# Performance work log

Hardware: AMD Instinct MI355X
Metric: run time of the kernel (lower is better)

## Reference

```python
import jax, jax.numpy as jnp
import numpy as np

N = 50000      # query points
M = 50000      # support points
KNN = 32       # neighbors per query
K = 15         # kernel points
C_IN = 64
C_OUT = 128
RADIUS = 2.5
KP_EXTENT = 1.2


def setup_inputs() -> dict:
    key = jax.random.key(0)
    ks = jax.random.split(key, 6)
    q_pts = jax.random.uniform(ks[0], (N, 3), dtype=jnp.float32)
    s_pts = jax.random.uniform(ks[1], (M, 3), dtype=jnp.float32)
    s_feats = jax.random.normal(ks[2], (M, C_IN), dtype=jnp.float32)
    # index M refers to the appended shadow point/feature row
    neigh_inds = jax.random.randint(ks[3], (N, KNN), 0, M + 1, dtype=jnp.int32)
    weights = jax.random.normal(ks[4], (K, C_IN, C_OUT), dtype=jnp.float32) * 0.05
    kernel_points = (jax.random.uniform(ks[5], (K, 3), dtype=jnp.float32) * 2.0 - 1.0) * RADIUS
    return {"q_pts": q_pts, "s_pts": s_pts, "s_feats": s_feats,
            "neigh_inds": neigh_inds, "weights": weights,
            "kernel_points": kernel_points}


def reference(q_pts, s_pts, s_feats, neigh_inds, weights, kernel_points):
    # append shadow point far away and zero shadow feature row
    s_pts_pad = jnp.concatenate([s_pts, jnp.full((1, 3), 1e6, s_pts.dtype)], axis=0)
    s_feats_pad = jnp.concatenate(
        [s_feats, jnp.zeros((1, s_feats.shape[1]), s_feats.dtype)], axis=0)

    neigh_pts = s_pts_pad[neigh_inds] - q_pts[:, None, :]       # (n, k, 3)
    neigh_feats = s_feats_pad[neigh_inds]                        # (n, k, c_in)

    diff = neigh_pts[:, :, None, :] - kernel_points[None, None]  # (n, k, K, 3)
    sq_dist = jnp.sum(diff * diff, axis=-1) + 1e-8               # (n, k, K)

    # linear kernel-point influence
    h = jnp.clip(1.0 - jnp.sqrt(sq_dist) / KP_EXTENT, 0.0)       # (n, k, K)

    # aggregate neighbor feats per kernel point, then apply per-kernel weights
    kernel_feats = jnp.einsum('nke,nkc->nec', h, neigh_feats)    # (n, K, c_in)
    q_feats = jnp.einsum('nec,eco->no', kernel_feats, weights)   # (n, c_out)

    # normalize by number of valid (non-shadow, sum>0) neighbors
    neighbor_num = jnp.sum(jnp.sum(neigh_feats, axis=-1) > 0, axis=-1)
    neighbor_num = jnp.maximum(neighbor_num, 1).astype(q_feats.dtype)[:, None]
    return q_feats / neighbor_num
```

## Files before the change

### kernel.cpp

```cpp
#include <hip/hip_runtime.h>


namespace {
constexpr int NQ   = 50000;
constexpr int MS   = 50000;
constexpr int KNN  = 32;
constexpr int KP   = 15;
constexpr int CIN  = 64;
constexpr int COUT = 128;
constexpr int QB   = 16;
constexpr int ROWS = KP * CIN;
constexpr int RND  = 3;
constexpr int RE   = 5;
constexpr int RROWS = RE * CIN;
constexpr int KBR  = RROWS / 32;
constexpr int KBT  = ROWS / 32;
constexpr int NT   = COUT / 16;
constexpr int ASTR = RROWS + 4;
constexpr float KP_EXT_INV = 1.0f / 1.2f;
constexpr size_t WS_HI  = 200704;
constexpr size_t WS_LO  = WS_HI + (size_t)ROWS * COUT * 2;
constexpr size_t WS_NEED = WS_LO + (size_t)ROWS * COUT * 2;
}

typedef __attribute__((ext_vector_type(8))) short short8;
typedef __attribute__((ext_vector_type(4))) float f32x4;

__device__ __forceinline__ short f32_bf16(float x) {
    unsigned u = __builtin_bit_cast(unsigned, x);
    u = u + 0x7fffu + ((u >> 16) & 1u);
    return (short)(u >> 16);
}
__device__ __forceinline__ float bf16_f32(short h) {
    unsigned u = ((unsigned)(unsigned short)h) << 16;
    return __builtin_bit_cast(float, u);
}

__global__ __launch_bounds__(256)
void rowsum_kernel(const float* __restrict__ s_feats, float* __restrict__ rs)
{
    int t = blockIdx.x * 256 + threadIdx.x;
    int row = t >> 3;
    int l8  = t & 7;
    if (row >= MS) return;
    const float4* p = (const float4*)(s_feats + (size_t)row * CIN + l8 * 8);
    float4 a = p[0], b = p[1];
    float s = ((a.x + a.y) + (a.z + a.w)) + ((b.x + b.y) + (b.z + b.w));
    s += __shfl_xor(s, 1);
    s += __shfl_xor(s, 2);
    s += __shfl_xor(s, 4);
    if (l8 == 0) rs[row] = s;
}

__global__ __launch_bounds__(256)
void wsplit_kernel(const float* __restrict__ W, short* __restrict__ whi, short* __restrict__ wlo)
{
    int tid = blockIdx.x * 256 + threadIdx.x;
    if (tid >= NT * KBT * 64 * 8) return;
    int j    = tid & 7;
    int lane = (tid >> 3) & 63;
    int kbt  = tid >> 9;
    int kb   = kbt % KBT;
    int t    = kbt / KBT;
    int row  = kb * 32 + ((lane >> 4) & 3) * 8 + j;
    int col  = t * 16 + (lane & 15);
    float x  = W[(size_t)row * COUT + col];
    short hi = f32_bf16(x);
    short lo = f32_bf16(x - bf16_f32(hi));
    whi[tid] = hi;
    wlo[tid] = lo;
}

__global__ __launch_bounds__(256, 4)
void kpconv_mfma(const float* __restrict__ q_pts,
                 const float* __restrict__ s_pts,
                 const float* __restrict__ s_feats,
                 const int*   __restrict__ neigh,
                 const float* __restrict__ kpts,
                 const float* __restrict__ rowsum,
                 const short* __restrict__ whi,
                 const short* __restrict__ wlo,
                 float*       __restrict__ out)
{
    __shared__ __align__(16) float smem[QB * ASTR];
    __shared__ float norm_s[QB];

    float (*h_lds)[KNN][20] = (float (*)[KNN][20])smem;
    float (*dxyz)[KNN][3]   = (float (*)[KNN][3])(smem + 2560);
    int*   idxl             = (int*)(smem + 2944);
    float* kp_s             = smem + 3072;

    const int tid  = threadIdx.x;
    const int lane = tid & 63;
    const int wv   = tid >> 6;
    const int blk  = blockIdx.x;
    const int k32  = lane & 31;
    const int half = lane >> 5;

    if (tid < KP * 3) kp_s[tid] = kpts[tid];
    __syncthreads();

    float kfv[4][KP];

    #pragma unroll
    for (int j = 0; j < 4; ++j) {
        const int q = wv * 4 + j;
        const int n = blk * QB + q;
        const float qx = q_pts[n * 3 + 0];
        const float qy = q_pts[n * 3 + 1];
        const float qz = q_pts[n * 3 + 2];

        bool flag = false;
        if (lane < KNN) {
            int idx = neigh[n * KNN + k32];
            idxl[wv * KNN + k32] = idx;
            bool valid = idx < MS;
            int  ic    = valid ? idx : MS - 1;
            float px = s_pts[ic * 3 + 0];
            float py = s_pts[ic * 3 + 1];
            float pz = s_pts[ic * 3 + 2];
            dxyz[wv][k32][0] = valid ? px - qx : 1e6f;
            dxyz[wv][k32][1] = valid ? py - qy : 1e6f;
            dxyz[wv][k32][2] = valid ? pz - qz : 1e6f;
            flag = valid && (rowsum[ic] > 0.0f);
        }
        {
            unsigned long long b = __ballot(flag);
            int cnt = (int)__popcll(b);
            if (lane == 0) norm_s[q] = 1.0f / (float)(cnt > 1 ? cnt : 1);
        }
        __builtin_amdgcn_wave_barrier();

        const float dx = dxyz[wv][k32][0];
        const float dy = dxyz[wv][k32][1];
        const float dz = dxyz[wv][k32][2];
        float om = 0.0f;
        #pragma unroll
        for (int p = 0; p < 8; ++p) {
            const int e = (p << 1) + half;
            if (e < KP) {
                float ax = dx - kp_s[e * 3 + 0];
                float ay = dy - kp_s[e * 3 + 1];
                float az = dz - kp_s[e * 3 + 2];
                float d2 = ax * ax + ay * ay + az * az + 1e-8f;
                float hh = 1.0f - sqrtf(d2) * KP_EXT_INV;
                hh = hh > 0.0f ? hh : 0.0f;
                h_lds[wv][k32][e] = hh;
                om = fmaxf(om, hh);
            }
        }
        om = fmaxf(om, __shfl_xor(om, 32));
        unsigned long long bh = __ballot(om > 0.0f);
        unsigned int kmask = (unsigned int)bh;
        __builtin_amdgcn_wave_barrier();

        #pragma unroll
        for (int e = 0; e < KP; ++e) kfv[j][e] = 0.0f;
        unsigned int mk = kmask;
        while (mk) {
            int k = __builtin_ctz(mk);
            mk &= mk - 1;
            int idx2 = idxl[wv * KNN + k];
            int ic2  = idx2 < MS ? idx2 : MS - 1;
            float nf = s_feats[(size_t)ic2 * CIN + lane];
            const float4* hr = (const float4*)(&h_lds[wv][k][0]);
            float4 h0 = hr[0], h1 = hr[1], h2 = hr[2], h3 = hr[3];
            kfv[j][0]  += h0.x * nf;  kfv[j][1]  += h0.y * nf;
            kfv[j][2]  += h0.z * nf;  kfv[j][3]  += h0.w * nf;
            kfv[j][4]  += h1.x * nf;  kfv[j][5]  += h1.y * nf;
            kfv[j][6]  += h1.z * nf;  kfv[j][7]  += h1.w * nf;
            kfv[j][8]  += h2.x * nf;  kfv[j][9]  += h2.y * nf;
            kfv[j][10] += h2.z * nf;  kfv[j][11] += h2.w * nf;
            kfv[j][12] += h3.x * nf;  kfv[j][13] += h3.y * nf;
            kfv[j][14] += h3.z * nf;
        }
    }

    const int qA   = lane & 15;
    const int quad = lane >> 4;
    const int t0 = 2 * wv, t1 = 2 * wv + 1;

    f32x4 acc0 = {0.f, 0.f, 0.f, 0.f};
    f32x4 acc1 = {0.f, 0.f, 0.f, 0.f};

    const short8* wh = (const short8*)whi;
    const short8* wl = (const short8*)wlo;

    #pragma unroll
    for (int r = 0; r < RND; ++r) {
        __syncthreads();
        #pragma unroll
        for (int j = 0; j < 4; ++j) {
            #pragma unroll
            for (int e5 = 0; e5 < RE; ++e5) {
                smem[(4 * wv + j) * ASTR + e5 * CIN + lane] = kfv[j][r * RE + e5];
            }
        }
        __syncthreads();

        #pragma unroll 2
        for (int kb = 0; kb < KBR; ++kb) {
            const float4* ap = (const float4*)(smem + qA * ASTR + kb * 32 + quad * 8);
            float4 a01 = ap[0], a23 = ap[1];
            float av[8] = {a01.x, a01.y, a01.z, a01.w, a23.x, a23.y, a23.z, a23.w};
            short8 ahi, alo;
            #pragma unroll
            for (int u = 0; u < 8; ++u) {
                short hi = f32_bf16(av[u]);
                ahi[u] = hi;
                alo[u] = f32_bf16(av[u] - bf16_f32(hi));
            }
            const int kbg = r * KBR + kb;
            short8 b0h = wh[(t0 * KBT + kbg) * 64 + lane];
            short8 b0l = wl[(t0 * KBT + kbg) * 64 + lane];
            short8 b1h = wh[(t1 * KBT + kbg) * 64 + lane];
            short8 b1l = wl[(t1 * KBT + kbg) * 64 + lane];

            acc0 = __builtin_amdgcn_mfma_f32_16x16x32_bf16(ahi, b0h, acc0, 0, 0, 0);
            acc0 = __builtin_amdgcn_mfma_f32_16x16x32_bf16(ahi, b0l, acc0, 0, 0, 0);
            acc0 = __builtin_amdgcn_mfma_f32_16x16x32_bf16(alo, b0h, acc0, 0, 0, 0);
            acc1 = __builtin_amdgcn_mfma_f32_16x16x32_bf16(ahi, b1h, acc1, 0, 0, 0);
            acc1 = __builtin_amdgcn_mfma_f32_16x16x32_bf16(ahi, b1l, acc1, 0, 0, 0);
            acc1 = __builtin_amdgcn_mfma_f32_16x16x32_bf16(alo, b1h, acc1, 0, 0, 0);
        }
    }

    const int oc = lane & 15;
    #pragma unroll
    for (int rr = 0; rr < 4; ++rr) {
        int qm = quad * 4 + rr;
        float nm = norm_s[qm];
        size_t rowb = (size_t)(blk * QB + qm) * COUT;
        out[rowb + t0 * 16 + oc] = acc0[rr] * nm;
        out[rowb + t1 * 16 + oc] = acc1[rr] * nm;
    }
}

__global__ __launch_bounds__(256, 6)
void kpconv_fallback(const float* __restrict__ q_pts,
                     const float* __restrict__ s_pts,
                     const float* __restrict__ s_feats,
                     const int*   __restrict__ neigh,
                     const float* __restrict__ W,
                     const float* __restrict__ kpts,
                     float*       __restrict__ out)
{
    constexpr int CHUNK_I = 320, NPAIR = 160;
    __shared__ __align__(16) float smem[NPAIR * 32];
    __shared__ float norm_s[QB];
    float (*h_lds)[KNN][20] = (float (*)[KNN][20])smem;
    float (*dxyz)[KNN][3]   = (float (*)[KNN][3])(smem + 2560);
    int*   idxl             = (int*)(smem + 2944);
    float* kp_s             = smem + 3072;

    const int tid = threadIdx.x, lane = tid & 63, wv = tid >> 6, blk = blockIdx.x;
    const int k32 = lane & 31, half = lane >> 5;
    if (tid < KP * 3) kp_s[tid] = kpts[tid];
    __syncthreads();
    float kfv[4][KP];

    #pragma unroll
    for (int j = 0; j < 4; ++j) {
        const int q = wv * 4 + j, n = blk * QB + q;
        const float qx = q_pts[n*3], qy = q_pts[n*3+1], qz = q_pts[n*3+2];
        if (lane < KNN) {
            int idx = neigh[n * KNN + k32];
            idxl[wv * KNN + k32] = idx;
            bool valid = idx < MS;
            int ic = valid ? idx : MS - 1;
            dxyz[wv][k32][0] = valid ? s_pts[ic*3]   - qx : 1e6f;
            dxyz[wv][k32][1] = valid ? s_pts[ic*3+1] - qy : 1e6f;
            dxyz[wv][k32][2] = valid ? s_pts[ic*3+2] - qz : 1e6f;
        }
        __builtin_amdgcn_wave_barrier();
        const float dx = dxyz[wv][k32][0], dy = dxyz[wv][k32][1], dz = dxyz[wv][k32][2];
        float om = 0.0f;
        #pragma unroll
        for (int p = 0; p < 8; ++p) {
            const int e = (p << 1) + half;
            if (e < KP) {
                float ax = dx - kp_s[e*3], ay = dy - kp_s[e*3+1], az = dz - kp_s[e*3+2];
                float hh = 1.0f - sqrtf(ax*ax + ay*ay + az*az + 1e-8f) * KP_EXT_INV;
                hh = hh > 0.0f ? hh : 0.0f;
                h_lds[wv][k32][e] = hh;
                om = fmaxf(om, hh);
            }
        }
        om = fmaxf(om, __shfl_xor(om, 32));
        unsigned int kmask = (unsigned int)__ballot(om > 0.0f);
        __builtin_amdgcn_wave_barrier();
        {
            int idx = idxl[wv * KNN + k32];
            bool valid = idx < MS;
            int ic = valid ? idx : MS - 1;
            const float4* rp = (const float4*)(s_feats + (size_t)ic * CIN + half * 32);
            float4 s4 = rp[0];
            #pragma unroll
            for (int t = 1; t < 8; ++t) { float4 a = rp[t]; s4.x+=a.x; s4.y+=a.y; s4.z+=a.z; s4.w+=a.w; }
            float s = (s4.x + s4.y) + (s4.z + s4.w);
            s += __shfl_xor(s, 32);
            unsigned long long b = __ballot(valid && (s > 0.0f));
            int cnt = (int)(__popcll(b) >> 1);
            if (lane == 0) norm_s[q] = 1.0f / (float)(cnt > 1 ? cnt : 1);
        }
        #pragma unroll
        for (int e = 0; e < KP; ++e) kfv[j][e] = 0.0f;
        unsigned int mk = kmask;
        while (mk) {
            int k = __builtin_ctz(mk); mk &= mk - 1;
            int idx2 = idxl[wv * KNN + k];
            int ic2 = idx2 < MS ? idx2 : MS - 1;
            float nf = s_feats[(size_t)ic2 * CIN + lane];
            const float4* hr = (const float4*)(&h_lds[wv][k][0]);
            float4 h0 = hr[0], h1 = hr[1], h2 = hr[2], h3 = hr[3];
            kfv[j][0]+=h0.x*nf; kfv[j][1]+=h0.y*nf; kfv[j][2]+=h0.z*nf; kfv[j][3]+=h0.w*nf;
            kfv[j][4]+=h1.x*nf; kfv[j][5]+=h1.y*nf; kfv[j][6]+=h1.z*nf; kfv[j][7]+=h1.w*nf;
            kfv[j][8]+=h2.x*nf; kfv[j][9]+=h2.y*nf; kfv[j][10]+=h2.z*nf; kfv[j][11]+=h2.w*nf;
            kfv[j][12]+=h3.x*nf; kfv[j][13]+=h3.y*nf; kfv[j][14]+=h3.z*nf;
        }
    }

    const int o4 = tid & 31, qi = tid >> 5, q0 = qi * 2, q1 = q0 + 1;
    float4 tot0 = make_float4(0,0,0,0), tot1 = make_float4(0,0,0,0);
    #pragma unroll
    for (int r = 0; r < 3; ++r) {
        __syncthreads();
        #pragma unroll
        for (int j = 0; j < 4; ++j) {
            const int q = wv * 4 + j;
            #pragma unroll
            for (int e5 = 0; e5 < 5; ++e5) {
                int i = e5 * CIN + lane, pr = i >> 1, m = pr & 14;
                smem[pr * 32 + ((q ^ m) << 1) + (i & 1)] = kfv[j][r * 5 + e5];
            }
        }
        __syncthreads();
        const float* wb = W + (size_t)(r * CHUNK_I) * COUT + (o4 << 2);
        float4 acc0 = make_float4(0,0,0,0), acc1 = make_float4(0,0,0,0);
        #pragma unroll 4
        for (int p = 0; p < NPAIR; ++p) {
            float4 kk = *(const float4*)(smem + p * 32 + ((q0 ^ (p & 14)) << 1));
            float4 w0 = *(const float4*)(wb + (size_t)(2*p) * COUT);
            float4 w1 = *(const float4*)(wb + (size_t)(2*p+1) * COUT);
            acc0.x+=w0.x*kk.x; acc0.y+=w0.y*kk.x; acc0.z+=w0.z*kk.x; acc0.w+=w0.w*kk.x;
            acc1.x+=w0.x*kk.z; acc1.y+=w0.y*kk.z; acc1.z+=w0.z*kk.z; acc1.w+=w0.w*kk.z;
            acc0.x+=w1.x*kk.y; acc0.y+=w1.y*kk.y; acc0.z+=w1.z*kk.y; acc0.w+=w1.w*kk.y;
            acc1.x+=w1.x*kk.w; acc1.y+=w1.y*kk.w; acc1.z+=w1.z*kk.w; acc1.w+=w1.w*kk.w;
        }
        tot0.x+=acc0.x; tot0.y+=acc0.y; tot0.z+=acc0.z; tot0.w+=acc0.w;
        tot1.x+=acc1.x; tot1.y+=acc1.y; tot1.z+=acc1.z; tot1.w+=acc1.w;
    }
    const float nm0 = norm_s[q0], nm1 = norm_s[q1];
    const size_t base = (size_t)(blk * QB) * COUT + (o4 << 2);
    *(float4*)(out + base + (size_t)q0 * COUT) =
        make_float4(tot0.x*nm0, tot0.y*nm0, tot0.z*nm0, tot0.w*nm0);
    *(float4*)(out + base + (size_t)q1 * COUT) =
        make_float4(tot1.x*nm1, tot1.y*nm1, tot1.z*nm1, tot1.w*nm1);
}

extern "C" void kernel_launch(void* const* d_in, const int* in_sizes, int n_in,
                              void* d_out, int out_size, void* d_ws, size_t ws_size,
                              hipStream_t stream) {
    const float* q_pts   = (const float*)d_in[0];
    const float* s_pts   = (const float*)d_in[1];
    const float* s_feats = (const float*)d_in[2];
    const int*   neigh   = (const int*)d_in[3];
    const float* W       = (const float*)d_in[4];
    const float* kpts    = (const float*)d_in[5];
    float* outp = (float*)d_out;

    dim3 grid(NQ / QB);
    dim3 block(256);

    if (ws_size >= WS_NEED) {
        float* rs  = (float*)d_ws;
        short* whi = (short*)((char*)d_ws + WS_HI);
        short* wlo = (short*)((char*)d_ws + WS_LO);
        int rs_blocks = (MS * 8 + 255) / 256;
        hipLaunchKernelGGL(rowsum_kernel, dim3(rs_blocks), dim3(256), 0, stream, s_feats, rs);
        hipLaunchKernelGGL(wsplit_kernel, dim3((NT * KBT * 64 * 8 + 255) / 256), dim3(256),
                           0, stream, W, whi, wlo);
        hipLaunchKernelGGL(kpconv_mfma, grid, block, 0, stream,
                           q_pts, s_pts, s_feats, neigh, kpts, rs, whi, wlo, outp);
    } else {
        hipLaunchKernelGGL(kpconv_fallback, grid, block, 0, stream,
                           q_pts, s_pts, s_feats, neigh, W, kpts, outp);
    }
}
```

Before: 173.1 us.

## Double query tile to 32 and reuse weight fragments across two MFMA row blocks

The main kernel now uses 512-thread blocks covering 32 queries. Each wave handles one 16-column output tile for two 16-query row blocks, so every loaded weight hi/lo fragment feeds two MFMAs and weight traffic per query is halved. Kernel features are split into bf16 hi/lo once when written to shared memory, with perm instructions unpacking them, instead of being re-split per MFMA read. The neighbor loop is replaced by a compacted list of valid neighbor indices whose feature loads are batched four at a time. The two prep kernels are merged into one launch. Costs are more shared memory and registers per block, which may lower occupancy, plus bounds guards for the partial last tile.

```diff
diff --git a/kernel.cpp b/kernel.cpp
--- a/kernel.cpp
+++ b/kernel.cpp
@@ -8,23 +8,27 @@
 constexpr int KP   = 15;
 constexpr int CIN  = 64;
 constexpr int COUT = 128;
-constexpr int QB   = 16;
+constexpr int QB   = 32;
 constexpr int ROWS = KP * CIN;
 constexpr int RND  = 3;
 constexpr int RE   = 5;
-constexpr int RROWS = RE * CIN;
-constexpr int KBR  = RROWS / 32;
+constexpr int KBR  = (RE * CIN) / 32;
 constexpr int KBT  = ROWS / 32;
 constexpr int NT   = COUT / 16;
-constexpr int ASTR = RROWS + 4;
+constexpr int ASTR = RE * CIN + 4;
 constexpr float KP_EXT_INV = 1.0f / 1.2f;
-constexpr size_t WS_HI  = 200704;
-constexpr size_t WS_LO  = WS_HI + (size_t)ROWS * COUT * 2;
+constexpr size_t WS_HI   = 200704;
+constexpr size_t WS_LO   = WS_HI + (size_t)ROWS * COUT * 2;
 constexpr size_t WS_NEED = WS_LO + (size_t)ROWS * COUT * 2;
+constexpr int OF_H   = 0;
+constexpr int OF_DX  = 5280;
+constexpr int OF_CPK = 6048;
+constexpr int OF_KP  = 6304;
 }
 
 typedef __attribute__((ext_vector_type(8))) short short8;
 typedef __attribute__((ext_vector_type(4))) float f32x4;
+typedef __attribute__((ext_vector_type(4))) unsigned int u32x4;
 
 __device__ __forceinline__ short f32_bf16(float x) {
     unsigned u = __builtin_bit_cast(unsigned, x);
@@ -35,43 +39,70 @@
     unsigned u = ((unsigned)(unsigned short)h) << 16;
     return __builtin_bit_cast(float, u);
 }
+__device__ __forceinline__ unsigned pack_hilo(float x) {
+    unsigned xu = __builtin_bit_cast(unsigned, x);
+    unsigned r  = xu + 0x7fffu + ((xu >> 16) & 1u);
+    unsigned hi = r & 0xffff0000u;
+    float lof = x - __builtin_bit_cast(float, hi);
+    unsigned lu = __builtin_bit_cast(unsigned, lof);
+    unsigned r2 = lu + 0x7fffu + ((lu >> 16) & 1u);
+    return hi | (r2 >> 16);
+}
+__device__ __forceinline__ unsigned permb(unsigned a, unsigned b, unsigned sel) {
+#if __has_builtin(__builtin_amdgcn_perm)
+    return __builtin_amdgcn_perm(a, b, sel);
+#else
+    if (sel == 0x07060302u) return (a & 0xffff0000u) | (b >> 16);
+    return (a << 16) | (b & 0xffffu);
+#endif
+}
+__device__ __forceinline__ void unpack_a(uint4 a, uint4 b, short8& hi, short8& lo) {
+    u32x4 h, l;
+    h[0] = permb(a.y, a.x, 0x07060302u); l[0] = permb(a.y, a.x, 0x05040100u);
+    h[1] = permb(a.w, a.z, 0x07060302u); l[1] = permb(a.w, a.z, 0x05040100u);
+    h[2] = permb(b.y, b.x, 0x07060302u); l[2] = permb(b.y, b.x, 0x05040100u);
+    h[3] = permb(b.w, b.z, 0x07060302u); l[3] = permb(b.w, b.z, 0x05040100u);
+    hi = __builtin_bit_cast(short8, h);
+    lo = __builtin_bit_cast(short8, l);
+}
 
 __global__ __launch_bounds__(256)
-void rowsum_kernel(const float* __restrict__ s_feats, float* __restrict__ rs)
+void prep_kernel(const float* __restrict__ s_feats, const float* __restrict__ W,
+                 float* __restrict__ rs, short* __restrict__ whi, short* __restrict__ wlo)
 {
-    int t = blockIdx.x * 256 + threadIdx.x;
-    int row = t >> 3;
-    int l8  = t & 7;
-    if (row >= MS) return;
-    const float4* p = (const float4*)(s_feats + (size_t)row * CIN + l8 * 8);
-    float4 a = p[0], b = p[1];
-    float s = ((a.x + a.y) + (a.z + a.w)) + ((b.x + b.y) + (b.z + b.w));
-    s += __shfl_xor(s, 1);
-    s += __shfl_xor(s, 2);
-    s += __shfl_xor(s, 4);
-    if (l8 == 0) rs[row] = s;
-}
-
-__global__ __launch_bounds__(256)
-void wsplit_kernel(const float* __restrict__ W, short* __restrict__ whi, short* __restrict__ wlo)
-{
-    int tid = blockIdx.x * 256 + threadIdx.x;
-    if (tid >= NT * KBT * 64 * 8) return;
-    int j    = tid & 7;
-    int lane = (tid >> 3) & 63;
-    int kbt  = tid >> 9;
-    int kb   = kbt % KBT;
-    int t    = kbt / KBT;
-    int row  = kb * 32 + ((lane >> 4) & 3) * 8 + j;
-    int col  = t * 16 + (lane & 15);
-    float x  = W[(size_t)row * COUT + col];
-    short hi = f32_bf16(x);
-    short lo = f32_bf16(x - bf16_f32(hi));
-    whi[tid] = hi;
-    wlo[tid] = lo;
-}
-
-__global__ __launch_bounds__(256, 4)
+    int b = blockIdx.x;
+    if (b < 60) {
+        int wv = threadIdx.x >> 6, lane = threadIdx.x & 63;
+        int id = b * 4 + wv;
+        int t = id / KBT, kb = id % KBT;
+        short8 hi8, lo8;
+        #pragma unroll
+        for (int j = 0; j < 8; ++j) {
+            int row = kb * 32 + ((lane >> 4) & 3) * 8 + j;
+            int col = t * 16 + (lane & 15);
+            float x = W[(size_t)row * COUT + col];
+            short h = f32_bf16(x);
+            hi8[j] = h;
+            lo8[j] = f32_bf16(x - bf16_f32(h));
+        }
+        ((short8*)whi)[id * 64 + lane] = hi8;
+        ((short8*)wlo)[id * 64 + lane] = lo8;
+    } else {
+        int tdx = (b - 60) * 256 + threadIdx.x;
+        int row = tdx >> 3, l8 = tdx & 7;
+        if (row < MS) {
+            const float4* p = (const float4*)(s_feats + (size_t)row * CIN + l8 * 8);
+            float4 a = p[0], c = p[1];
+            float s = ((a.x + a.y) + (a.z + a.w)) + ((c.x + c.y) + (c.z + c.w));
+            s += __shfl_xor(s, 1);
+            s += __shfl_xor(s, 2);
+            s += __shfl_xor(s, 4);
+            if (l8 == 0) rs[row] = s;
+        }
+    }
+}
+
+__global__ __launch_bounds__(512, 4)
 void kpconv_mfma(const float* __restrict__ q_pts,
                  const float* __restrict__ s_pts,
                  const float* __restrict__ s_feats,
@@ -82,46 +113,50 @@
                  const short* __restrict__ wlo,
                  float*       __restrict__ out)
 {
-    __shared__ __align__(16) float smem[QB * ASTR];
+    __shared__ __align__(16) unsigned int smem[QB * ASTR];
     __shared__ float norm_s[QB];
 
-    float (*h_lds)[KNN][20] = (float (*)[KNN][20])smem;
-    float (*dxyz)[KNN][3]   = (float (*)[KNN][3])(smem + 2560);
-    int*   idxl             = (int*)(smem + 2944);
-    float* kp_s             = smem + 3072;
-
+    float* smf   = (float*)smem;
     const int tid  = threadIdx.x;
     const int lane = tid & 63;
     const int wv   = tid >> 6;
     const int blk  = blockIdx.x;
     const int k32  = lane & 31;
     const int half = lane >> 5;
+    const int quad = lane >> 4;
+
+    float* hbase = smf + OF_H + wv * 660;
+    float* dx_b  = smf + OF_DX + wv * 96;
+    int*   cpk   = (int*)(smf + OF_CPK) + wv * 32;
+    float* kp_s  = smf + OF_KP;
 
     if (tid < KP * 3) kp_s[tid] = kpts[tid];
+    if (lane < 20) hbase[640 + lane] = 0.0f;
     __syncthreads();
 
     float kfv[4][KP];
 
     #pragma unroll
     for (int j = 0; j < 4; ++j) {
-        const int q = wv * 4 + j;
-        const int n = blk * QB + q;
-        const float qx = q_pts[n * 3 + 0];
-        const float qy = q_pts[n * 3 + 1];
-        const float qz = q_pts[n * 3 + 2];
-
+        const int q  = wv * 4 + j;
+        const int n  = blk * QB + q;
+        const int nc = n < NQ ? n : NQ - 1;
+        const float qx = q_pts[nc * 3 + 0];
+        const float qy = q_pts[nc * 3 + 1];
+        const float qz = q_pts[nc * 3 + 2];
+
+        int idx = MS;
         bool flag = false;
         if (lane < KNN) {
-            int idx = neigh[n * KNN + k32];
-            idxl[wv * KNN + k32] = idx;
+            idx = neigh[nc * KNN + k32];
             bool valid = idx < MS;
             int  ic    = valid ? idx : MS - 1;
             float px = s_pts[ic * 3 + 0];
             float py = s_pts[ic * 3 + 1];
             float pz = s_pts[ic * 3 + 2];
-            dxyz[wv][k32][0] = valid ? px - qx : 1e6f;
-            dxyz[wv][k32][1] = valid ? py - qy : 1e6f;
-            dxyz[wv][k32][2] = valid ? pz - qz : 1e6f;
+            dx_b[k32 * 3 + 0] = valid ? px - qx : 1e6f;
+            dx_b[k32 * 3 + 1] = valid ? py - qy : 1e6f;
+            dx_b[k32 * 3 + 2] = valid ? pz - qz : 1e6f;
             flag = valid && (rowsum[ic] > 0.0f);
         }
         {
@@ -131,9 +166,9 @@
         }
         __builtin_amdgcn_wave_barrier();
 
-        const float dx = dxyz[wv][k32][0];
-        const float dy = dxyz[wv][k32][1];
-        const float dz = dxyz[wv][k32][2];
+        const float dx = dx_b[k32 * 3 + 0];
+        const float dy = dx_b[k32 * 3 + 1];
+        const float dz = dx_b[k32 * 3 + 2];
         float om = 0.0f;
         #pragma unroll
         for (int p = 0; p < 8; ++p) {
@@ -145,94 +180,100 @@
                 float d2 = ax * ax + ay * ay + az * az + 1e-8f;
                 float hh = 1.0f - sqrtf(d2) * KP_EXT_INV;
                 hh = hh > 0.0f ? hh : 0.0f;
-                h_lds[wv][k32][e] = hh;
+                hbase[k32 * 20 + e] = hh;
                 om = fmaxf(om, hh);
             }
         }
         om = fmaxf(om, __shfl_xor(om, 32));
-        unsigned long long bh = __ballot(om > 0.0f);
-        unsigned int kmask = (unsigned int)bh;
+        unsigned int kmask = (unsigned int)__ballot(om > 0.0f);
+        int nv = __popc(kmask);
+
+        if (lane < KNN) {
+            bool bit = (kmask >> k32) & 1u;
+            int pos = bit ? __popc(kmask & ((1u << k32) - 1u))
+                          : nv + __popc((~kmask) & ((1u << k32) - 1u));
+            cpk[pos] = bit ? ((idx << 6) | k32) : 32;
+        }
         __builtin_amdgcn_wave_barrier();
 
         #pragma unroll
         for (int e = 0; e < KP; ++e) kfv[j][e] = 0.0f;
-        unsigned int mk = kmask;
-        while (mk) {
-            int k = __builtin_ctz(mk);
-            mk &= mk - 1;
-            int idx2 = idxl[wv * KNN + k];
-            int ic2  = idx2 < MS ? idx2 : MS - 1;
-            float nf = s_feats[(size_t)ic2 * CIN + lane];
-            const float4* hr = (const float4*)(&h_lds[wv][k][0]);
-            float4 h0 = hr[0], h1 = hr[1], h2 = hr[2], h3 = hr[3];
-            kfv[j][0]  += h0.x * nf;  kfv[j][1]  += h0.y * nf;
-            kfv[j][2]  += h0.z * nf;  kfv[j][3]  += h0.w * nf;
-            kfv[j][4]  += h1.x * nf;  kfv[j][5]  += h1.y * nf;
-            kfv[j][6]  += h1.z * nf;  kfv[j][7]  += h1.w * nf;
-            kfv[j][8]  += h2.x * nf;  kfv[j][9]  += h2.y * nf;
-            kfv[j][10] += h2.z * nf;  kfv[j][11] += h2.w * nf;
-            kfv[j][12] += h3.x * nf;  kfv[j][13] += h3.y * nf;
-            kfv[j][14] += h3.z * nf;
-        }
-    }
-
-    const int qA   = lane & 15;
-    const int quad = lane >> 4;
-    const int t0 = 2 * wv, t1 = 2 * wv + 1;
-
+        const int nvr = (nv + 3) & ~3;
+        for (int base = 0; base < nvr; base += 4) {
+            int pk[4];
+            float nf[4];
+            #pragma unroll
+            for (int u = 0; u < 4; ++u) pk[u] = __builtin_amdgcn_readfirstlane(cpk[base + u]);
+            #pragma unroll
+            for (int u = 0; u < 4; ++u) nf[u] = s_feats[(size_t)(pk[u] >> 6) * CIN + lane];
+            #pragma unroll
+            for (int u = 0; u < 4; ++u) {
+                const float4* hr = (const float4*)(hbase + (pk[u] & 63) * 20);
+                float4 h0 = hr[0], h1 = hr[1], h2 = hr[2], h3 = hr[3];
+                float f = nf[u];
+                kfv[j][0]  += h0.x * f;  kfv[j][1]  += h0.y * f;
+                kfv[j][2]  += h0.z * f;  kfv[j][3]  += h0.w * f;
+                kfv[j][4]  += h1.x * f;  kfv[j][5]  += h1.y * f;
+                kfv[j][6]  += h1.z * f;  kfv[j][7]  += h1.w * f;
+                kfv[j][8]  += h2.x * f;  kfv[j][9]  += h2.y * f;
+                kfv[j][10] += h2.z * f;  kfv[j][11] += h2.w * f;
+                kfv[j][12] += h3.x * f;  kfv[j][13] += h3.y * f;
+                kfv[j][14] += h3.z * f;
+            }
+        }
+    }
+
+    const short8* wh = (const short8*)whi;
+    const short8* wl = (const short8*)wlo;
     f32x4 acc0 = {0.f, 0.f, 0.f, 0.f};
     f32x4 acc1 = {0.f, 0.f, 0.f, 0.f};
-
-    const short8* wh = (const short8*)whi;
-    const short8* wl = (const short8*)wlo;
+    const int qA = lane & 15;
 
     #pragma unroll
     for (int r = 0; r < RND; ++r) {
         __syncthreads();
         #pragma unroll
         for (int j = 0; j < 4; ++j) {
+            const int q = wv * 4 + j;
             #pragma unroll
             for (int e5 = 0; e5 < RE; ++e5) {
-                smem[(4 * wv + j) * ASTR + e5 * CIN + lane] = kfv[j][r * RE + e5];
+                smem[q * ASTR + e5 * CIN + lane] = pack_hilo(kfv[j][r * RE + e5]);
             }
         }
         __syncthreads();
 
         #pragma unroll 2
         for (int kb = 0; kb < KBR; ++kb) {
-            const float4* ap = (const float4*)(smem + qA * ASTR + kb * 32 + quad * 8);
-            float4 a01 = ap[0], a23 = ap[1];
-            float av[8] = {a01.x, a01.y, a01.z, a01.w, a23.x, a23.y, a23.z, a23.w};
-            short8 ahi, alo;
-            #pragma unroll
-            for (int u = 0; u < 8; ++u) {
-                short hi = f32_bf16(av[u]);
-                ahi[u] = hi;
-                alo[u] = f32_bf16(av[u] - bf16_f32(hi));
-            }
+            const uint4* a0p = (const uint4*)(smem + qA * ASTR + kb * 32 + quad * 8);
+            uint4 a0 = a0p[0], a0b = a0p[1];
+            const uint4* a1p = (const uint4*)(smem + (16 + qA) * ASTR + kb * 32 + quad * 8);
+            uint4 a1 = a1p[0], a1b = a1p[1];
+            short8 ah0, al0, ah1, al1;
+            unpack_a(a0, a0b, ah0, al0);
+            unpack_a(a1, a1b, ah1, al1);
+
             const int kbg = r * KBR + kb;
-            short8 b0h = wh[(t0 * KBT + kbg) * 64 + lane];
-            short8 b0l = wl[(t0 * KBT + kbg) * 64 + lane];
-            short8 b1h = wh[(t1 * KBT + kbg) * 64 + lane];
-            short8 b1l = wl[(t1 * KBT + kbg) * 64 + lane];
-
-            acc0 = __builtin_amdgcn_mfma_f32_16x16x32_bf16(ahi, b0h, acc0, 0, 0, 0);
-            acc0 = __builtin_amdgcn_mfma_f32_16x16x32_bf16(ahi, b0l, acc0, 0, 0, 0);
-            acc0 = __builtin_amdgcn_mfma_f32_16x16x32_bf16(alo, b0h, acc0, 0, 0, 0);
-            acc1 = __builtin_amdgcn_mfma_f32_16x16x32_bf16(ahi, b1h, acc1, 0, 0, 0);
-            acc1 = __builtin_amdgcn_mfma_f32_16x16x32_bf16(ahi, b1l, acc1, 0, 0, 0);
-            acc1 = __builtin_amdgcn_mfma_f32_16x16x32_bf16(alo, b1h, acc1, 0, 0, 0);
+            short8 bh = wh[(wv * KBT + kbg) * 64 + lane];
+            short8 bl = wl[(wv * KBT + kbg) * 64 + lane];
+
+            acc0 = __builtin_amdgcn_mfma_f32_16x16x32_bf16(ah0, bh, acc0, 0, 0, 0);
+            acc1 = __builtin_amdgcn_mfma_f32_16x16x32_bf16(ah1, bh, acc1, 0, 0, 0);
+            acc0 = __builtin_amdgcn_mfma_f32_16x16x32_bf16(ah0, bl, acc0, 0, 0, 0);
+            acc1 = __builtin_amdgcn_mfma_f32_16x16x32_bf16(ah1, bl, acc1, 0, 0, 0);
+            acc0 = __builtin_amdgcn_mfma_f32_16x16x32_bf16(al0, bh, acc0, 0, 0, 0);
+            acc1 = __builtin_amdgcn_mfma_f32_16x16x32_bf16(al1, bh, acc1, 0, 0, 0);
         }
     }
 
     const int oc = lane & 15;
     #pragma unroll
     for (int rr = 0; rr < 4; ++rr) {
-        int qm = quad * 4 + rr;
-        float nm = norm_s[qm];
-        size_t rowb = (size_t)(blk * QB + qm) * COUT;
-        out[rowb + t0 * 16 + oc] = acc0[rr] * nm;
-        out[rowb + t1 * 16 + oc] = acc1[rr] * nm;
+        int qm0 = quad * 4 + rr;
+        int qm1 = 16 + qm0;
+        int n0 = blk * QB + qm0;
+        int n1 = blk * QB + qm1;
+        if (n0 < NQ) out[(size_t)n0 * COUT + wv * 16 + oc] = acc0[rr] * norm_s[qm0];
+        if (n1 < NQ) out[(size_t)n1 * COUT + wv * 16 + oc] = acc1[rr] * norm_s[qm1];
     }
 }
 
@@ -245,9 +286,9 @@
                      const float* __restrict__ kpts,
                      float*       __restrict__ out)
 {
-    constexpr int CHUNK_I = 320, NPAIR = 160;
+    constexpr int QBF = 16, CHUNK_I = 320, NPAIR = 160;
     __shared__ __align__(16) float smem[NPAIR * 32];
-    __shared__ float norm_s[QB];
+    __shared__ float norm_s[QBF];
     float (*h_lds)[KNN][20] = (float (*)[KNN][20])smem;
     float (*dxyz)[KNN][3]   = (float (*)[KNN][3])(smem + 2560);
     int*   idxl             = (int*)(smem + 2944);
@@ -261,7 +302,7 @@
 
     #pragma unroll
     for (int j = 0; j < 4; ++j) {
-        const int q = wv * 4 + j, n = blk * QB + q;
+        const int q = wv * 4 + j, n = blk * QBF + q;
         const float qx = q_pts[n*3], qy = q_pts[n*3+1], qz = q_pts[n*3+2];
         if (lane < KNN) {
             int idx = neigh[n * KNN + k32];
@@ -351,7 +392,7 @@
         tot1.x+=acc1.x; tot1.y+=acc1.y; tot1.z+=acc1.z; tot1.w+=acc1.w;
     }
     const float nm0 = norm_s[q0], nm1 = norm_s[q1];
-    const size_t base = (size_t)(blk * QB) * COUT + (o4 << 2);
+    const size_t base = (size_t)(blk * QBF) * COUT + (o4 << 2);
     *(float4*)(out + base + (size_t)q0 * COUT) =
         make_float4(tot0.x*nm0, tot0.y*nm0, tot0.z*nm0, tot0.w*nm0);
     *(float4*)(out + base + (size_t)q1 * COUT) =
@@ -369,21 +410,17 @@
     const float* kpts    = (const float*)d_in[5];
     float* outp = (float*)d_out;
 
-    dim3 grid(NQ / QB);
-    dim3 block(256);
-
     if (ws_size >= WS_NEED) {
         float* rs  = (float*)d_ws;
         short* whi = (short*)((char*)d_ws + WS_HI);
         short* wlo = (short*)((char*)d_ws + WS_LO);
         int rs_blocks = (MS * 8 + 255) / 256;
-        hipLaunchKernelGGL(rowsum_kernel, dim3(rs_blocks), dim3(256), 0, stream, s_feats, rs);
-        hipLaunchKernelGGL(wsplit_kernel, dim3((NT * KBT * 64 * 8 + 255) / 256), dim3(256),
-                           0, stream, W, whi, wlo);
-        hipLaunchKernelGGL(kpconv_mfma, grid, block, 0, stream,
+        hipLaunchKernelGGL(prep_kernel, dim3(60 + rs_blocks), dim3(256), 0, stream,
+                           s_feats, W, rs, whi, wlo);
+        hipLaunchKernelGGL(kpconv_mfma, dim3((NQ + QB - 1) / QB), dim3(512), 0, stream,
                            q_pts, s_pts, s_feats, neigh, kpts, rs, whi, wlo, outp);
     } else {
-        hipLaunchKernelGGL(kpconv_fallback, grid, block, 0, stream,
+        hipLaunchKernelGGL(kpconv_fallback, dim3(NQ / 16), dim3(256), 0, stream,
                            q_pts, s_pts, s_feats, neigh, W, kpts, outp);
     }
 }
```

Result: faster. 163.8 us (-5.3%).
